# Kernel tuning notes

Hardware: AMD Instinct MI355X
Metric: run time of the kernel (lower is better)

## Reference

```python
import jax, jax.numpy as jnp
import numpy as np
import math

N, E, T, H, IN_DIM, G, L = 8192, 131072, 262144, 128, 64, 32, 2
RBF_BINS, RBF_MAX, ANG_BINS = 32, 5.0, 16


def _rbf(d, r_max, n_bins):
    centers = jnp.linspace(0.0, r_max, n_bins, dtype=jnp.float32)
    delta = r_max / max(n_bins - 1, 1)
    gamma = 1.0 / (2.0 * (delta ** 2 + 1e-12))
    diff = d[:, None] - centers[None, :]
    return jnp.exp(-gamma * diff * diff)


def _mlp2(x, w1, b1, w2, b2):
    return jax.nn.silu(x @ w1 + b1) @ w2 + b2


def _ln(x, g, b):
    mu = jnp.mean(x, -1, keepdims=True)
    var = jnp.mean((x - mu) ** 2, -1, keepdims=True)
    return (x - mu) * jax.lax.rsqrt(var + 1e-5) * g + b


def _safe_norm(v):
    # ||v|| with grad-safe sqrt at v=0
    return jnp.sqrt(jnp.sum(v * v, -1) + 1e-12)


def setup_inputs() -> dict:
    key = jax.random.key(0)
    ks = iter(jax.random.split(key, 64))

    def lin(fan_in, shape):
        return jax.random.normal(next(ks), shape, jnp.float32) * (fan_in ** -0.5)

    x = jax.random.normal(next(ks), (N, IN_DIM), jnp.float32)
    pos = jax.random.normal(next(ks), (N, 3), jnp.float32) * 2.0
    edge_index = jax.random.randint(next(ks), (2, E), 0, N, jnp.int32)
    edge_dist = jnp.linalg.norm(pos[edge_index[1]] - pos[edge_index[0]], axis=-1)
    triplet_kj = jax.random.randint(next(ks), (T,), 0, E, jnp.int32)
    triplet_ji = jax.random.randint(next(ks), (T,), 0, E, jnp.int32)
    batch = jnp.sort(jax.random.randint(next(ks), (N,), 0, G, jnp.int32))
    TM_IN, MM_IN, CTX = 2 * RBF_BINS + ANG_BINS, 3 * H + RBF_BINS, 3 * H
    d = dict(
        x=x, pos=pos, edge_dist=edge_dist,
        node_in_w=lin(IN_DIM, (IN_DIM, H)), node_in_b=jnp.zeros(H),
        tm_w1=lin(TM_IN, (L, TM_IN, H)), tm_b1=jnp.zeros((L, H)),
        tm_w2=lin(H, (L, H, H)), tm_b2=jnp.zeros((L, H)),
        mm_w1=lin(MM_IN, (L, MM_IN, H)), mm_b1=jnp.zeros((L, H)),
        mm_w2=lin(H, (L, H, 2 * H)), mm_b2=jnp.zeros((L, 2 * H)),
        us_w1=lin(CTX, (L, CTX, H)), us_b1=jnp.zeros((L, H)),
        us_w2=lin(H, (L, H, H)), us_b2=jnp.zeros((L, H)),
        gv_w1=lin(CTX, (L, CTX, H)), gv_b1=jnp.zeros((L, H)),
        gv_w2=lin(H, (L, H, H)), gv_b2=jnp.zeros((L, H)),
        ln_g=jnp.ones((L, H)), ln_b=jnp.zeros((L, H)),
        vn_init=jnp.zeros(H),
        v2n_w1=lin(H, (H, H)), v2n_b1=jnp.zeros(H),
        v2n_w2=lin(H, (H, H)), v2n_b2=jnp.zeros(H),
        n2v_w1=lin(H, (H, H)), n2v_b1=jnp.zeros(H),
        n2v_w2=lin(H, (H, H)), n2v_b2=jnp.zeros(H),
        head_w1=lin(5 * H, (5 * H, H)), head_b1=jnp.zeros(H),
        head_w2=lin(H, (H, 1)), head_b2=jnp.zeros(1),
        edge_index=edge_index, triplet_kj=triplet_kj,
        triplet_ji=triplet_ji, batch=batch,
    )
    return d


def reference(x, pos, edge_dist, node_in_w, node_in_b, tm_w1, tm_b1, tm_w2, tm_b2,
              mm_w1, mm_b1, mm_w2, mm_b2, us_w1, us_b1, us_w2, us_b2,
              gv_w1, gv_b1, gv_w2, gv_b2, ln_g, ln_b, vn_init,
              v2n_w1, v2n_b1, v2n_w2, v2n_b2, n2v_w1, n2v_b1, n2v_w2, n2v_b2,
              head_w1, head_b1, head_w2, head_b2,
              edge_index, triplet_kj, triplet_ji, batch):
    src, dst = edge_index[0], edge_index[1]
    s = x @ node_in_w + node_in_b                              # [N,H]
    v = jnp.zeros((N, H, 3), s.dtype)                          # [N,H,3]
    vec = pos[dst] - pos[src]                                  # [E,3]
    edge_dir = vec / (edge_dist[:, None] + 1e-9)               # [E,3]
    edge_rbf = _rbf(edge_dist, RBF_MAX, RBF_BINS)              # [E,32]
    # 3-body angles between edge ji and edge kj
    a, b = vec[triplet_ji], vec[triplet_kj]                    # [T,3]
    cos = jnp.sum(a * b, -1) / (_safe_norm(a) * _safe_norm(b) + 1e-9)
    angle = jnp.arccos(jnp.clip(cos, -1.0 + 1e-7, 1.0 - 1e-7))
    angle_feat = _rbf(angle, math.pi, ANG_BINS)                # [T,16]
    vn = jnp.broadcast_to(vn_init, (G, H))
    for l in range(L):
        s = s + _mlp2(vn, v2n_w1, v2n_b1, v2n_w2, v2n_b2)[batch]
        # triplet gather -> MLP -> scatter onto edges
        t_in = jnp.concatenate([edge_rbf[triplet_kj], edge_rbf[triplet_ji], angle_feat], -1)
        t_msg = _mlp2(t_in, tm_w1[l], tm_b1[l], tm_w2[l], tm_b2[l])
        angle_agg = jax.ops.segment_sum(t_msg, triplet_ji, num_segments=E)   # [E,H]
        # edge messages -> scatter onto nodes (scalar + vector channels)
        msg_in = jnp.concatenate([s[src], s[dst], edge_rbf, angle_agg], -1)  # [E,416]
        msg = _mlp2(msg_in, mm_w1[l], mm_b1[l], mm_w2[l], mm_b2[l])          # [E,2H]
        m_s, m_vc = msg[:, :H], msg[:, H:]
        agg_s = jax.ops.segment_sum(m_s, dst, num_segments=N)                # [N,H]
        m_v = m_vc[:, :, None] * edge_dir[:, None, :]                        # [E,H,3]
        agg_v = jax.ops.segment_sum(m_v.reshape(E, H * 3), dst, num_segments=N).reshape(N, H, 3)
        ctx = jnp.concatenate([s, agg_s, _safe_norm(v)], -1)                 # [N,3H]
        s = s + _mlp2(ctx, us_w1[l], us_b1[l], us_w2[l], us_b2[l])
        gate = jax.nn.sigmoid(_mlp2(ctx, gv_w1[l], gv_b1[l], gv_w2[l], gv_b2[l]))
        v = v + gate[:, :, None] * agg_v
        s = jax.nn.silu(_ln(s, ln_g[l], ln_b[l]))
        vn = vn + _mlp2(jax.ops.segment_sum(s, batch, num_segments=G),
                        n2v_w1, n2v_b1, n2v_w2, n2v_b2)
    nf = jnp.concatenate([s, _safe_norm(v)], -1)                             # [N,2H]
    add_p = jax.ops.segment_sum(nf, batch, num_segments=G)
    counts = jax.ops.segment_sum(jnp.ones((N,), nf.dtype), batch, num_segments=G)
    mean_p = add_p / jnp.maximum(counts, 1.0)[:, None]
    g = jnp.concatenate([add_p, mean_p, vn], -1)                             # [G,5H]
    pred = _mlp2(g, head_w1, head_b1, head_w2, head_b2)                      # [G,1]
    return pred[:, 0]
```

## Files before the change

kernel.cpp:

```cpp
#include <hip/hip_runtime.h>
#include <math.h>

#define N_   8192
#define E_   131072
#define T_   262144
#define H_   128
#define IND_ 64
#define G_   32
#define L_   2

#define CW 64
#define RB 16

#define MROWS 32
#define HSTRIDE 136
#define WSTRIDE 36

#define STEP_E  ((float)(5.0/31.0))
#define GAMMA_E ((float)(1.0/(2.0*((5.0/31.0)*(5.0/31.0) + 1e-12))))
#define PI_D    3.14159265358979323846
#define STEP_A  ((float)(PI_D/15.0))
#define GAMMA_A ((float)(1.0/(2.0*((PI_D/15.0)*(PI_D/15.0) + 1e-12))))

typedef __attribute__((ext_vector_type(8))) short short8;
typedef __attribute__((ext_vector_type(4))) float f32x4;
typedef unsigned short ushort_t;

static __device__ __forceinline__ float silu_f(float x){ return x / (1.f + expf(-x)); }
static __device__ __forceinline__ float sigmoid_f(float x){ return 1.f / (1.f + expf(-x)); }

static __device__ __forceinline__ ushort_t f2bf(float x){
  unsigned int u = __builtin_bit_cast(unsigned int, x);
  u += 0x7FFFu + ((u >> 16) & 1u);
  return (ushort_t)(u >> 16);
}
static __device__ __forceinline__ float bf2f(ushort_t h){
  unsigned int u = ((unsigned int)h) << 16;
  return __builtin_bit_cast(float, u);
}


__global__ void k_zero(float* __restrict__ p, long n){
  long stride = (long)gridDim.x*256;
  long n4 = n >> 2;
  float4* p4 = (float4*)p;
  for (long i = (long)blockIdx.x*256 + threadIdx.x; i < n4; i += stride)
    p4[i] = make_float4(0.f,0.f,0.f,0.f);
  for (long i = (n4<<2) + (long)blockIdx.x*256 + threadIdx.x; i < n; i += stride)
    p[i] = 0.f;
}

__global__ void k_sentinel(float* __restrict__ p, int n){
  int i = blockIdx.x*256 + threadIdx.x;
  if (i < n) p[i] = 1.0e30f;
}

__global__ void k_init_vn(float* __restrict__ vn, const float* __restrict__ vn_init){
  int i = blockIdx.x*256 + threadIdx.x;
  if (i < G_*H_) vn[i] = vn_init[i & 127];
}

__global__ void k_bhist(const int* __restrict__ batch, int* __restrict__ bh){
  int i = blockIdx.x*256 + threadIdx.x;
  if (i < N_) atomicAdd(&bh[batch[i]], 1);
}
__global__ void k_bscan(int* __restrict__ bh){
  if (threadIdx.x == 0 && blockIdx.x == 0){
    int a = 0;
    for (int g=0; g<G_; g++){ a += bh[g]; bh[g] = a; }
  }
}

__global__ void k_wt_all(const float* __restrict__ tm_w1, const float* __restrict__ tm_w2,
                         const float* __restrict__ mm_w1, const float* __restrict__ mm_w2,
                         const float* __restrict__ us_w1, const float* __restrict__ us_w2,
                         const float* __restrict__ gv_w1, const float* __restrict__ gv_w2,
                         ushort_t* __restrict__ wtbuf){
  const int l = blockIdx.y;
  int i = blockIdx.x*256 + threadIdx.x;
  if (i >= 245760) return;
  ushort_t* base = wtbuf + (size_t)l*376832;
  if (i < 12288){
    int c = i/96, k = i%96;
    base[i] = (k < 80) ? f2bf(tm_w1[(size_t)l*10240 + (size_t)k*128 + c]) : (ushort_t)0;
  } else if (i < 28672){
    int j = i - 12288; int c = j >> 7, k = j & 127;
    base[12288 + j] = f2bf(tm_w2[(size_t)l*16384 + (size_t)k*128 + c]);
  } else if (i < 81920){
    int j = i - 28672; int c = j/416, k = j%416;
    base[28672 + j] = f2bf(mm_w1[(size_t)l*53248 + (size_t)k*128 + c]);
  } else if (i < 114688){
    int j = i - 81920; int c = j >> 7, k = j & 127;
    base[81920 + j] = f2bf(mm_w2[(size_t)l*32768 + (size_t)k*256 + c]);
  } else if (i < 163840){
    int j = i - 114688; int c = j/384, k = j%384;
    float w = us_w1[(size_t)l*49152 + (size_t)k*128 + c];
    ushort_t h = f2bf(w);
    base[114688 + j] = h; base[163840 + j] = f2bf(w - bf2f(h));
  } else if (i < 180224){
    int j = i - 163840; int c = j >> 7, k = j & 127;
    float w = us_w2[(size_t)l*16384 + (size_t)k*128 + c];
    ushort_t h = f2bf(w);
    base[212992 + j] = h; base[229376 + j] = f2bf(w - bf2f(h));
  } else if (i < 229376){
    int j = i - 180224; int c = j/384, k = j%384;
    float w = gv_w1[(size_t)l*49152 + (size_t)k*128 + c];
    ushort_t h = f2bf(w);
    base[245760 + j] = h; base[294912 + j] = f2bf(w - bf2f(h));
  } else {
    int j = i - 229376; int c = j >> 7, k = j & 127;
    float w = gv_w2[(size_t)l*16384 + (size_t)k*128 + c];
    ushort_t h = f2bf(w);
    base[344064 + j] = h; base[360448 + j] = f2bf(w - bf2f(h));
  }
}

__global__ void k_geom(const float* __restrict__ pos, const float* __restrict__ dist,
                       const int* __restrict__ ei,
                       float* __restrict__ vec, float* __restrict__ dir,
                       ushort_t* __restrict__ rbf16){
  int e = blockIdx.x*256 + threadIdx.x;
  if (e >= E_) return;
  int s = ei[e], d = ei[E_ + e];
  float vx = pos[d*3+0] - pos[s*3+0];
  float vy = pos[d*3+1] - pos[s*3+1];
  float vz = pos[d*3+2] - pos[s*3+2];
  vec[e*3+0]=vx; vec[e*3+1]=vy; vec[e*3+2]=vz;
  float dd = dist[e];
  float inv = 1.f / (dd + 1e-9f);
  dir[e*3+0]=vx*inv; dir[e*3+1]=vy*inv; dir[e*3+2]=vz*inv;
  #pragma unroll
  for (int i=0;i<32;i++){
    float df = dd - i*STEP_E;
    rbf16[e*32+i] = f2bf(expf(-GAMMA_E*df*df));
  }
}

__global__ void k_dirs(const float* __restrict__ dir, const int* __restrict__ perm_e,
                       float* __restrict__ dir_s){
  int p = blockIdx.x*256 + threadIdx.x;
  if (p >= E_) return;
  int e = perm_e[p];
  dir_s[p*3+0] = dir[e*3+0];
  dir_s[p*3+1] = dir[e*3+1];
  dir_s[p*3+2] = dir[e*3+2];
}

__global__ void k_angle(const float* __restrict__ vec,
                        const int* __restrict__ kj, const int* __restrict__ ji,
                        float* __restrict__ angle){
  int t = blockIdx.x*256 + threadIdx.x;
  if (t >= T_) return;
  int ea = ji[t], eb = kj[t];
  float ax=vec[ea*3+0], ay=vec[ea*3+1], az=vec[ea*3+2];
  float bx=vec[eb*3+0], by=vec[eb*3+1], bz=vec[eb*3+2];
  float dot = ax*bx + ay*by + az*bz;
  float na = sqrtf(ax*ax+ay*ay+az*az + 1e-12f);
  float nb = sqrtf(bx*bx+by*by+bz*bz + 1e-12f);
  float c = dot / (na*nb + 1e-9f);
  c = fminf(fmaxf(c, -1.f + 1e-7f), 1.f - 1e-7f);
  angle[t] = acosf(c);
}


__global__ void k_hist(const int* __restrict__ keys, int M, int* __restrict__ hist){
  int i = blockIdx.x*256 + threadIdx.x;
  if (i < M) atomicAdd(&hist[keys[i]], 1);
}

__global__ void k_hist2(const int* __restrict__ keys, const int* __restrict__ map,
                        int M, int* __restrict__ hist){
  int i = blockIdx.x*256 + threadIdx.x;
  if (i < M) atomicAdd(&hist[map[keys[i]]], 1);
}

__global__ void k_scan1(const int* __restrict__ in, int* __restrict__ out,
                        int* __restrict__ sums, int B){
  __shared__ int sh[1024];
  int base = blockIdx.x*1024, t = threadIdx.x;
  for (int j=t;j<1024;j+=256) sh[j] = (base+j<B) ? in[base+j] : 0;
  __syncthreads();
  for (int o=1;o<1024;o<<=1){
    int v[4];
    #pragma unroll
    for (int q=0;q<4;q++){ int idx=t+q*256; v[q]=(idx>=o)? sh[idx-o]:0; }
    __syncthreads();
    #pragma unroll
    for (int q=0;q<4;q++){ int idx=t+q*256; sh[idx]+=v[q]; }
    __syncthreads();
  }
  for (int j=t;j<1024;j+=256) if (base+j<B) out[base+j] = (j==0)?0:sh[j-1];
  if (t==0) sums[blockIdx.x] = sh[1023];
}

__global__ void k_scan2(int* __restrict__ sums, int nb){
  if (threadIdx.x==0 && blockIdx.x==0){
    int a=0;
    for (int i=0;i<nb;i++){ int x=sums[i]; sums[i]=a; a+=x; }
  }
}

__global__ void k_scan3(int* __restrict__ out, const int* __restrict__ sums, int B){
  int i = blockIdx.x*256+threadIdx.x;
  if (i<B) out[i] += sums[i>>10];
}

__global__ void k_fill(const int* __restrict__ keys, int M, int* __restrict__ cur,
                       int* __restrict__ perm){
  int i = blockIdx.x*256+threadIdx.x;
  if (i<M){ int p = atomicAdd(&cur[keys[i]],1); perm[p]=i; }
}

__global__ void k_fill2(const int* __restrict__ keys, const int* __restrict__ map,
                        int M, int* __restrict__ cur, int* __restrict__ perm){
  int i = blockIdx.x*256+threadIdx.x;
  if (i<M){ int p = atomicAdd(&cur[map[keys[i]]],1); perm[p]=i; }
}

__global__ void k_invert(const int* __restrict__ perm, int* __restrict__ rank, int M){
  int i = blockIdx.x*256+threadIdx.x;
  if (i<M) rank[perm[i]] = i;
}

template<int SM, int K1PAD>
__launch_bounds__(256, 3)
__global__ void k_mlp1(
    const int* __restrict__ perm,
    const int* __restrict__ idx1, const int* __restrict__ idx2,
    const ushort_t* __restrict__ rbf16, const float* __restrict__ angle,
    const ushort_t* __restrict__ s16, const ushort_t* __restrict__ eagg_in,
    const ushort_t* __restrict__ W1t, const float* __restrict__ b1,
    ushort_t* __restrict__ outbuf)
{
  __shared__ ushort_t lw[128*WSTRIDE];
  __shared__ ushort_t hid[4*MROWS*HSTRIDE];
  const int tid  = threadIdx.x;
  const int wave = tid >> 6;
  const int lane = tid & 63;
  const int n    = lane & 15;
  const int quad = lane >> 4;
  const int kq   = quad*8;
  const int wrow = blockIdx.x*128 + wave*MROWS;
  ushort_t* myhid = hid + wave*MROWS*HSTRIDE;

  const int e0 = perm[wrow + n];
  const int e1 = perm[wrow + 16 + n];

  int i1a = idx1[e0], i1b = idx1[e1];
  int i2a = idx2[e0], i2b = idx2[e1];
  float ang0 = 0.f, ang1 = 0.f;
  if (SM == 1){ ang0 = angle[e0]; ang1 = angle[e1]; }

  f32x4 acc[2][8];
  #pragma unroll
  for (int rh=0;rh<2;rh++)
    #pragma unroll
    for (int ct=0;ct<8;ct++) acc[rh][ct] = (f32x4){0.f,0.f,0.f,0.f};

  #pragma unroll
  for (int k0 = 0; k0 < K1PAD; k0 += 32){
    #pragma unroll
    for (int it=0; it<2; it++){
      int idx = tid + it*256;
      int col = idx >> 2, seg = idx & 3;
      *(short8*)&lw[col*WSTRIDE + seg*8] = *(const short8*)&W1t[(size_t)col*K1PAD + k0 + seg*8];
    }
    __syncthreads();

    short8 a0, a1;
    if (SM == 1){
      if (k0 == 0){
        a0 = *(const short8*)&rbf16[(size_t)i1a*32 + kq];
        a1 = *(const short8*)&rbf16[(size_t)i1b*32 + kq];
      } else if (k0 == 32){
        a0 = *(const short8*)&rbf16[(size_t)i2a*32 + kq];
        a1 = *(const short8*)&rbf16[(size_t)i2b*32 + kq];
      } else {
        #pragma unroll
        for (int j=0;j<8;j++){
          int kk = kq + j;
          float v0 = 0.f, v1 = 0.f;
          if (kk < 16){
            float c = (float)kk*STEP_A;
            float d0 = ang0 - c, d1 = ang1 - c;
            v0 = expf(-GAMMA_A*d0*d0); v1 = expf(-GAMMA_A*d1*d1);
          }
          a0[j] = (short)f2bf(v0); a1[j] = (short)f2bf(v1);
        }
      }
    } else {
      const int k = k0 + kq;
      if (k0 < 128){
        a0 = *(const short8*)&s16[(size_t)i1a*128 + k];
        a1 = *(const short8*)&s16[(size_t)i1b*128 + k];
      } else if (k0 < 256){
        a0 = *(const short8*)&s16[(size_t)i2a*128 + (k-128)];
        a1 = *(const short8*)&s16[(size_t)i2b*128 + (k-128)];
      } else if (k0 < 288){
        a0 = *(const short8*)&rbf16[(size_t)e0*32 + (k-256)];
        a1 = *(const short8*)&rbf16[(size_t)e1*32 + (k-256)];
      } else {
        a0 = *(const short8*)&eagg_in[(size_t)(wrow + n)*128 + (k-288)];
        a1 = *(const short8*)&eagg_in[(size_t)(wrow + 16 + n)*128 + (k-288)];
      }
    }
    #pragma unroll
    for (int ct=0;ct<8;ct++){
      short8 b = *(const short8*)&lw[(ct*16 + n)*WSTRIDE + kq];
      acc[0][ct] = __builtin_amdgcn_mfma_f32_16x16x32_bf16(a0, b, acc[0][ct], 0,0,0);
      acc[1][ct] = __builtin_amdgcn_mfma_f32_16x16x32_bf16(a1, b, acc[1][ct], 0,0,0);
    }
    __syncthreads();
  }

  #pragma unroll
  for (int rh=0;rh<2;rh++){
    #pragma unroll
    for (int ct=0;ct<8;ct++){
      int col = ct*16 + n;
      float bv = b1[col];
      #pragma unroll
      for (int reg=0;reg<4;reg++){
        int rloc = rh*16 + quad*4 + reg;
        float h = acc[rh][ct][reg] + bv;
        myhid[rloc*HSTRIDE + col] = f2bf(silu_f(h));
      }
    }
  }
  const int rsub = lane >> 4;
  const int c8   = (lane & 15) * 8;
  #pragma unroll
  for (int i=0;i<8;i++){
    int rloc = i*4 + rsub;
    int grow = wrow + rloc;
    short8 vv = *(const short8*)&myhid[(size_t)rloc*HSTRIDE + c8];
    *(short8*)&outbuf[(size_t)grow*128 + c8] = vv;
  }
}

__global__ void k_agg_t(const ushort_t* __restrict__ tmsg, const int* __restrict__ tends,
                        ushort_t* __restrict__ eagg2){
  int i = blockIdx.x*256 + threadIdx.x;
  int r = i >> 6, c2 = (i & 63)*2;
  if (r >= E_) return;
  int s = (r == 0) ? 0 : tends[r-1];
  int e = tends[r];
  float a0 = 0.f, a1 = 0.f;
  for (int p=s;p<e;p++){
    unsigned int w = *(const unsigned int*)&tmsg[(size_t)p*128 + c2];
    a0 += bf2f((ushort_t)(w & 0xFFFFu));
    a1 += bf2f((ushort_t)(w >> 16));
  }
  unsigned int o = (unsigned int)f2bf(a0) | ((unsigned int)f2bf(a1) << 16);
  *(unsigned int*)&eagg2[(size_t)r*128 + c2] = o;
}

__global__ void k_agg_e(const ushort_t* __restrict__ hbuf, const int* __restrict__ eends,
                        const float* __restrict__ dir_s, float* __restrict__ mom){
  int i = blockIdx.x*256 + threadIdx.x;
  int d = i >> 6, c2 = (i & 63)*2;
  if (d >= N_) return;
  int s = (d == 0) ? 0 : eends[d-1];
  int e = eends[d];
  float hs0=0.f,hs1=0.f, hx0=0.f,hx1=0.f, hy0=0.f,hy1=0.f, hz0=0.f,hz1=0.f;
  float sdx=0.f, sdy=0.f, sdz=0.f;
  for (int q=s;q<e;q++){
    unsigned int w = *(const unsigned int*)&hbuf[(size_t)q*128 + c2];
    float h0 = bf2f((ushort_t)(w & 0xFFFFu));
    float h1 = bf2f((ushort_t)(w >> 16));
    float dx = dir_s[q*3+0], dy = dir_s[q*3+1], dz = dir_s[q*3+2];
    hs0 += h0; hs1 += h1;
    hx0 += h0*dx; hx1 += h1*dx;
    hy0 += h0*dy; hy1 += h1*dy;
    hz0 += h0*dz; hz1 += h1*dz;
    sdx += dx; sdy += dy; sdz += dz;
  }
  size_t base = (size_t)d*128 + c2;
  *(float2*)&mom[base]                        = make_float2(hs0, hs1);
  *(float2*)&mom[(size_t)N_*128   + base]     = make_float2(hx0, hx1);
  *(float2*)&mom[(size_t)N_*256   + base]     = make_float2(hy0, hy1);
  *(float2*)&mom[(size_t)N_*384   + base]     = make_float2(hz0, hz1);
  if (c2 == 0){
    mom[(size_t)N_*512 + d*4+0] = sdx;
    mom[(size_t)N_*512 + d*4+1] = sdy;
    mom[(size_t)N_*512 + d*4+2] = sdz;
  }
}

__launch_bounds__(64, 4)
__global__ void k_gemm_t(ushort_t* __restrict__ eagg2, const int* __restrict__ tends,
                         const ushort_t* __restrict__ W2t, const float* __restrict__ b2){
  __shared__ ushort_t hid[MROWS*HSTRIDE];
  const int lane = threadIdx.x;
  const int n    = lane & 15;
  const int quad = lane >> 4;
  const int kq   = quad*8;
  const int wrow = blockIdx.x*MROWS;

  f32x4 acc[2][8];
  #pragma unroll
  for (int rh=0;rh<2;rh++)
    #pragma unroll
    for (int ct=0;ct<8;ct++) acc[rh][ct] = (f32x4){0.f,0.f,0.f,0.f};

  #pragma unroll
  for (int k0=0;k0<128;k0+=32){
    short8 a0 = *(const short8*)&eagg2[(size_t)(wrow + n)*128 + k0 + kq];
    short8 a1 = *(const short8*)&eagg2[(size_t)(wrow + 16 + n)*128 + k0 + kq];
    #pragma unroll
    for (int ct=0;ct<8;ct++){
      short8 b = *(const short8*)&W2t[(size_t)(ct*16 + n)*128 + k0 + kq];
      acc[0][ct] = __builtin_amdgcn_mfma_f32_16x16x32_bf16(a0, b, acc[0][ct], 0,0,0);
      acc[1][ct] = __builtin_amdgcn_mfma_f32_16x16x32_bf16(a1, b, acc[1][ct], 0,0,0);
    }
  }

  float cnts[2][4];
  #pragma unroll
  for (int rh=0;rh<2;rh++)
    #pragma unroll
    for (int reg=0;reg<4;reg++){
      int row = wrow + rh*16 + quad*4 + reg;
      cnts[rh][reg] = (float)(tends[row] - (row ? tends[row-1] : 0));
    }

  #pragma unroll
  for (int rh=0;rh<2;rh++){
    #pragma unroll
    for (int ct=0;ct<8;ct++){
      int col = ct*16 + n;
      float bv = b2[col];
      #pragma unroll
      for (int reg=0;reg<4;reg++){
        int rloc = rh*16 + quad*4 + reg;
        hid[rloc*HSTRIDE + col] = f2bf(acc[rh][ct][reg] + cnts[rh][reg]*bv);
      }
    }
  }
  const int rsub = lane >> 4;
  const int c8   = (lane & 15) * 8;
  #pragma unroll
  for (int i=0;i<8;i++){
    int rloc = i*4 + rsub;
    int grow = wrow + rloc;
    short8 vv = *(const short8*)&hid[(size_t)rloc*HSTRIDE + c8];
    *(short8*)&eagg2[(size_t)grow*128 + c8] = vv;
  }
}

__launch_bounds__(64, 4)
__global__ void k_gemm_e(const float* __restrict__ mom, const int* __restrict__ eends,
                         const ushort_t* __restrict__ W2t ,
                         const float* __restrict__ b2 ,
                         const float* __restrict__ v ,
                         ushort_t* __restrict__ a16h, ushort_t* __restrict__ a16l,
                         ushort_t* __restrict__ vnh,  ushort_t* __restrict__ vnl,
                         float* __restrict__ aggv ){
  __shared__ float sbuf[MROWS*130];
  const int lane = threadIdx.x;
  const int n    = lane & 15;
  const int quad = lane >> 4;
  const int kq   = quad*8;
  const int wrow = blockIdx.x*MROWS;
  const int og   = blockIdx.y;

  const float* M = mom + (size_t)og*((size_t)N_*128);
  const ushort_t* W = W2t + (og ? (size_t)128*128 : 0);

  f32x4 acc[2][8];
  #pragma unroll
  for (int rh=0;rh<2;rh++)
    #pragma unroll
    for (int ct=0;ct<8;ct++) acc[rh][ct] = (f32x4){0.f,0.f,0.f,0.f};

  #pragma unroll
  for (int k0=0;k0<128;k0+=32){
    const int k = k0 + kq;
    const float* p0 = &M[(size_t)(wrow + n)*128 + k];
    const float* p1 = &M[(size_t)(wrow + 16 + n)*128 + k];
    f32x4 x0 = *(const f32x4*)p0, x1 = *(const f32x4*)(p0+4);
    f32x4 y0 = *(const f32x4*)p1, y1 = *(const f32x4*)(p1+4);
    short8 ah0, al0, ah1, al1;
    #pragma unroll
    for (int j=0;j<4;j++){
      ushort_t h;
      h = f2bf(x0[j]); ah0[j]   = (short)h; al0[j]   = (short)f2bf(x0[j] - bf2f(h));
      h = f2bf(x1[j]); ah0[4+j] = (short)h; al0[4+j] = (short)f2bf(x1[j] - bf2f(h));
      h = f2bf(y0[j]); ah1[j]   = (short)h; al1[j]   = (short)f2bf(y0[j] - bf2f(h));
      h = f2bf(y1[j]); ah1[4+j] = (short)h; al1[4+j] = (short)f2bf(y1[j] - bf2f(h));
    }
    #pragma unroll
    for (int ct=0;ct<8;ct++){
      short8 b = *(const short8*)&W[(size_t)(ct*16 + n)*128 + k0 + kq];
      acc[0][ct] = __builtin_amdgcn_mfma_f32_16x16x32_bf16(ah0, b, acc[0][ct], 0,0,0);
      acc[0][ct] = __builtin_amdgcn_mfma_f32_16x16x32_bf16(al0, b, acc[0][ct], 0,0,0);
      acc[1][ct] = __builtin_amdgcn_mfma_f32_16x16x32_bf16(ah1, b, acc[1][ct], 0,0,0);
      acc[1][ct] = __builtin_amdgcn_mfma_f32_16x16x32_bf16(al1, b, acc[1][ct], 0,0,0);
    }
  }

  const int rsub = lane >> 4;
  const int c8   = (lane & 15) * 8;

  if (og == 0){
    float cnts[2][4];
    #pragma unroll
    for (int rh=0;rh<2;rh++)
      #pragma unroll
      for (int reg=0;reg<4;reg++){
        int row = wrow + rh*16 + quad*4 + reg;
        cnts[rh][reg] = (float)(eends[row] - (row ? eends[row-1] : 0));
      }
    ushort_t* us = (ushort_t*)sbuf;
    #pragma unroll
    for (int rh=0;rh<2;rh++)
      #pragma unroll
      for (int ct=0;ct<8;ct++){
        int col = ct*16 + n;
        float bv = b2[col];
        #pragma unroll
        for (int reg=0;reg<4;reg++){
          int rloc = rh*16 + quad*4 + reg;
          float val = acc[rh][ct][reg] + cnts[rh][reg]*bv;
          us[rloc*HSTRIDE + col] = f2bf(val);
        }
      }
    #pragma unroll
    for (int i=0;i<8;i++){
      int rloc = i*4 + rsub;
      short8 vv = *(const short8*)&us[(size_t)rloc*HSTRIDE + c8];
      *(short8*)&a16h[(size_t)(wrow + rloc)*128 + c8] = vv;
    }
    #pragma unroll
    for (int rh=0;rh<2;rh++)
      #pragma unroll
      for (int ct=0;ct<8;ct++){
        int col = ct*16 + n;
        float bv = b2[col];
        #pragma unroll
        for (int reg=0;reg<4;reg++){
          int rloc = rh*16 + quad*4 + reg;
          float val = acc[rh][ct][reg] + cnts[rh][reg]*bv;
          ushort_t h = f2bf(val);
          us[rloc*HSTRIDE + col] = f2bf(val - bf2f(h));
        }
      }
    #pragma unroll
    for (int i=0;i<8;i++){
      int rloc = i*4 + rsub;
      short8 vv = *(const short8*)&us[(size_t)rloc*HSTRIDE + c8];
      *(short8*)&a16l[(size_t)(wrow + rloc)*128 + c8] = vv;
    }
    #pragma unroll 4
    for (int j=0;j<32;j++){
      size_t idx = (size_t)wrow*128 + (size_t)j*128 + lane*2;
      float2 a = *(const float2*)&v[idx];
      float2 b = *(const float2*)&v[(size_t)N_*128 + idx];
      float2 c = *(const float2*)&v[(size_t)N_*256 + idx];
      float n0 = sqrtf(a.x*a.x + b.x*b.x + c.x*c.x + 1e-12f);
      float n1 = sqrtf(a.y*a.y + b.y*b.y + c.y*c.y + 1e-12f);
      ushort_t h0 = f2bf(n0), h1 = f2bf(n1);
      *(unsigned int*)&vnh[idx] = (unsigned int)h0 | ((unsigned int)h1 << 16);
      *(unsigned int*)&vnl[idx] = (unsigned int)f2bf(n0 - bf2f(h0))
                                | ((unsigned int)f2bf(n1 - bf2f(h1)) << 16);
    }
  } else {
    const int x = og - 1;
    #pragma unroll
    for (int rh=0;rh<2;rh++)
      #pragma unroll
      for (int ct=0;ct<8;ct++){
        int col = ct*16 + n;
        float bv = b2[128 + col];
        #pragma unroll
        for (int reg=0;reg<4;reg++){
          int rloc = rh*16 + quad*4 + reg;
          int row = wrow + rloc;
          float sd = mom[(size_t)N_*512 + row*4 + x];
          sbuf[rloc*130 + col] = acc[rh][ct][reg] + sd*bv;
        }
      }
    float* plane = aggv + (size_t)x*((size_t)N_*128);
    #pragma unroll
    for (int i=0;i<8;i++){
      int rloc = i*4 + rsub;
      f32x4 v0 = *(const f32x4*)&sbuf[rloc*130 + c8];
      f32x4 v1 = *(const f32x4*)&sbuf[rloc*130 + c8 + 4];
      *(f32x4*)&plane[(size_t)(wrow + rloc)*128 + c8] = v0;
      *(f32x4*)&plane[(size_t)(wrow + rloc)*128 + c8 + 4] = v1;
    }
  }
}

__launch_bounds__(256, 3)
__global__ void k_node_mfma(
    const float* __restrict__ s_in,
    const ushort_t* __restrict__ a16h, const ushort_t* __restrict__ a16l,
    const ushort_t* __restrict__ vnh,  const ushort_t* __restrict__ vnl,
    float* __restrict__ s2, float* __restrict__ v_out ,
    const float* __restrict__ aggv ,
    const ushort_t* __restrict__ us1h, const ushort_t* __restrict__ us1l, const float* __restrict__ us_b1,
    const ushort_t* __restrict__ us2h, const ushort_t* __restrict__ us2l, const float* __restrict__ us_b2,
    const ushort_t* __restrict__ gv1h, const ushort_t* __restrict__ gv1l, const float* __restrict__ gv_b1,
    const ushort_t* __restrict__ gv2h, const ushort_t* __restrict__ gv2l, const float* __restrict__ gv_b2)
{
  __shared__ ushort_t lwh[128*WSTRIDE];
  __shared__ ushort_t lwl[128*WSTRIDE];
  __shared__ ushort_t hidh[4][16*HSTRIDE];
  __shared__ ushort_t hidl[4][16*HSTRIDE];
  const int tid  = threadIdx.x;
  const int wave = tid >> 6;
  const int lane = tid & 63;
  const int n    = lane & 15;
  const int quad = lane >> 4;
  const int kq   = quad*8;
  const int og   = blockIdx.y;
  const int wrow = blockIdx.x*64 + wave*16;
  const int r0 = wrow + n;

  const ushort_t* W1h = og ? gv1h : us1h;
  const ushort_t* W1l = og ? gv1l : us1l;
  const float*    B1  = og ? gv_b1 : us_b1;
  const ushort_t* W2h = og ? gv2h : us2h;
  const ushort_t* W2l = og ? gv2l : us2l;
  const float*    B2  = og ? gv_b2 : us_b2;

  f32x4 acc[8];
  #pragma unroll
  for (int ct=0;ct<8;ct++) acc[ct] = (f32x4){0.f,0.f,0.f,0.f};

  #pragma unroll
  for (int k0=0; k0<384; k0+=32){
    #pragma unroll
    for (int it = 0; it < 2; it++){
      int idx = tid + it*256;
      int col = idx >> 2, seg = idx & 3;
      *(short8*)&lwh[col*WSTRIDE + seg*8] = *(const short8*)&W1h[(size_t)col*384 + k0 + seg*8];
      *(short8*)&lwl[col*WSTRIDE + seg*8] = *(const short8*)&W1l[(size_t)col*384 + k0 + seg*8];
    }
    __syncthreads();

    short8 ah0, al0;
    const int k = k0 + kq;
    if (k0 < 128){
      const float* p0 = &s_in[(size_t)r0*128 + k];
      f32x4 x0 = *(const f32x4*)p0, x1 = *(const f32x4*)(p0+4);
      #pragma unroll
      for (int j=0;j<4;j++){
        ushort_t h;
        h = f2bf(x0[j]); ah0[j]   = (short)h; al0[j]   = (short)f2bf(x0[j] - bf2f(h));
        h = f2bf(x1[j]); ah0[4+j] = (short)h; al0[4+j] = (short)f2bf(x1[j] - bf2f(h));
      }
    } else if (k0 < 256){
      int kk = k - 128;
      ah0 = *(const short8*)&a16h[(size_t)r0*128 + kk];
      al0 = *(const short8*)&a16l[(size_t)r0*128 + kk];
    } else {
      int kk = k - 256;
      ah0 = *(const short8*)&vnh[(size_t)r0*128 + kk];
      al0 = *(const short8*)&vnl[(size_t)r0*128 + kk];
    }
    #pragma unroll
    for (int ct=0;ct<8;ct++){
      short8 bh = *(const short8*)&lwh[(ct*16 + n)*WSTRIDE + kq];
      short8 bl = *(const short8*)&lwl[(ct*16 + n)*WSTRIDE + kq];
      acc[ct] = __builtin_amdgcn_mfma_f32_16x16x32_bf16(ah0, bh, acc[ct], 0,0,0);
      acc[ct] = __builtin_amdgcn_mfma_f32_16x16x32_bf16(al0, bh, acc[ct], 0,0,0);
      acc[ct] = __builtin_amdgcn_mfma_f32_16x16x32_bf16(ah0, bl, acc[ct], 0,0,0);
    }
    __syncthreads();
  }

  #pragma unroll
  for (int ct=0;ct<8;ct++){
    int col = ct*16 + n;
    float bv = B1[col];
    #pragma unroll
    for (int reg=0;reg<4;reg++){
      int rloc = quad*4 + reg;
      float h = silu_f(acc[ct][reg] + bv);
      ushort_t hh = f2bf(h);
      hidh[wave][rloc*HSTRIDE + col] = hh;
      hidl[wave][rloc*HSTRIDE + col] = f2bf(h - bf2f(hh));
    }
  }

  f32x4 acc2[8];
  #pragma unroll
  for (int ct=0;ct<8;ct++) acc2[ct] = (f32x4){0.f,0.f,0.f,0.f};

  #pragma unroll
  for (int k0=0;k0<128;k0+=32){
    #pragma unroll
    for (int it = 0; it < 2; it++){
      int idx = tid + it*256;
      int col = idx >> 2, seg = idx & 3;
      *(short8*)&lwh[col*WSTRIDE + seg*8] = *(const short8*)&W2h[(size_t)col*128 + k0 + seg*8];
      *(short8*)&lwl[col*WSTRIDE + seg*8] = *(const short8*)&W2l[(size_t)col*128 + k0 + seg*8];
    }
    __syncthreads();

    short8 ah0 = *(const short8*)&hidh[wave][(size_t)(n)*HSTRIDE + k0 + kq];
    short8 al0 = *(const short8*)&hidl[wave][(size_t)(n)*HSTRIDE + k0 + kq];
    #pragma unroll
    for (int ct=0;ct<8;ct++){
      short8 bh = *(const short8*)&lwh[(ct*16 + n)*WSTRIDE + kq];
      short8 bl = *(const short8*)&lwl[(ct*16 + n)*WSTRIDE + kq];
      acc2[ct] = __builtin_amdgcn_mfma_f32_16x16x32_bf16(ah0, bh, acc2[ct], 0,0,0);
      acc2[ct] = __builtin_amdgcn_mfma_f32_16x16x32_bf16(al0, bh, acc2[ct], 0,0,0);
      acc2[ct] = __builtin_amdgcn_mfma_f32_16x16x32_bf16(ah0, bl, acc2[ct], 0,0,0);
    }
    __syncthreads();
  }

  if (og == 0){
    #pragma unroll
    for (int ct=0;ct<8;ct++){
      int col = ct*16 + n;
      float bv = B2[col];
      #pragma unroll
      for (int reg=0;reg<4;reg++){
        int row = wrow + quad*4 + reg;
        size_t idx = (size_t)row*128 + col;
        s2[idx] = s_in[idx] + acc2[ct][reg] + bv;
      }
    }
  } else {
    #pragma unroll
    for (int ct=0;ct<8;ct++){
      int col = ct*16 + n;
      float bv = B2[col];
      #pragma unroll
      for (int reg=0;reg<4;reg++){
        int row = wrow + quad*4 + reg;
        size_t idx = (size_t)row*128 + col;
        float g = sigmoid_f(acc2[ct][reg] + bv);
        v_out[idx]                    += g*aggv[idx];
        v_out[(size_t)N_*128 + idx]   += g*aggv[(size_t)N_*128 + idx];
        v_out[(size_t)N_*256 + idx]   += g*aggv[(size_t)N_*256 + idx];
      }
    }
  }
}

__launch_bounds__(128)
__global__ void k_gemm(const float* __restrict__ A,
                       const float* __restrict__ W,
                       const float* __restrict__ bias,
                       float* __restrict__ C, int R, int K)
{
  __shared__ float ws[CW*128];
  __shared__ float as[RB][CW];
  const int tid = threadIdx.x;
  const int nchunk = (K + CW - 1) / CW;

  for (int rb = blockIdx.x*RB; rb < R; rb += gridDim.x*RB){
    float acc[RB];
    #pragma unroll
    for (int r=0;r<RB;r++) acc[r] = 0.f;

    for (int c=0;c<nchunk;c++){
      const int k0 = c*CW;
      for (int i=tid; i<CW*128; i+=128){
        int kk = i >> 7, col = i & 127;
        int k = k0 + kk;
        ws[i] = (k < K) ? W[k*128 + col] : 0.f;
      }
      for (int i=tid; i<RB*CW; i+=128){
        int r  = i >> 6, kk = i & 63;
        int k  = k0 + kk;
        as[r][kk] = (k < K) ? A[(long)(rb+r)*K + k] : 0.f;
      }
      __syncthreads();
      #pragma unroll 4
      for (int kq2=0; kq2<CW/4; kq2++){
        float w0 = ws[(4*kq2+0)*128 + tid];
        float w1 = ws[(4*kq2+1)*128 + tid];
        float w2 = ws[(4*kq2+2)*128 + tid];
        float w3 = ws[(4*kq2+3)*128 + tid];
        #pragma unroll
        for (int r=0;r<RB;r++){
          const float4 av = *reinterpret_cast<const float4*>(&as[r][4*kq2]);
          acc[r] = fmaf(av.x, w0, acc[r]);
          acc[r] = fmaf(av.y, w1, acc[r]);
          acc[r] = fmaf(av.z, w2, acc[r]);
          acc[r] = fmaf(av.w, w3, acc[r]);
        }
      }
      __syncthreads();
    }

    const float bv = bias[tid];
    #pragma unroll
    for (int r=0;r<RB;r++)
      C[(long)(rb+r)*128 + tid] = acc[r] + bv;
  }
}


__launch_bounds__(256)
__global__ void k_small_mlp2(const float* __restrict__ in,
                             const float* __restrict__ w1, const float* __restrict__ b1,
                             const float* __restrict__ w2, const float* __restrict__ b2,
                             float* __restrict__ outp, int accumulate){
  __shared__ float a[32][128];
  __shared__ float h[32][128];
  int tid = threadIdx.x;
  for (int i=tid;i<32*128;i+=256) a[i>>7][i&127] = in[i];
  __syncthreads();
  int col = tid & 127, rg = tid >> 7;
  float acc[16];
  #pragma unroll
  for (int r=0;r<16;r++) acc[r]=0.f;
  for (int k=0;k<128;k++){
    float w = w1[k*128+col];
    #pragma unroll
    for (int r=0;r<16;r++) acc[r] = fmaf(a[rg*16+r][k], w, acc[r]);
  }
  {
    float bv = b1[col];
    #pragma unroll
    for (int r=0;r<16;r++) h[rg*16+r][col] = silu_f(acc[r]+bv);
  }
  __syncthreads();
  #pragma unroll
  for (int r=0;r<16;r++) acc[r]=0.f;
  for (int k=0;k<128;k++){
    float w = w2[k*128+col];
    #pragma unroll
    for (int r=0;r<16;r++) acc[r] = fmaf(h[rg*16+r][k], w, acc[r]);
  }
  {
    float bv = b2[col];
    #pragma unroll
    for (int r=0;r<16;r++){
      int idx = (rg*16+r)*128+col;
      float val = acc[r]+bv;
      outp[idx] = accumulate ? outp[idx]+val : val;
    }
  }
}

__global__ void k_head(const float* __restrict__ gbuf,
                       const float* __restrict__ w1, const float* __restrict__ b1,
                       const float* __restrict__ w2, const float* __restrict__ b2,
                       float* __restrict__ outp){
  __shared__ float red[128];
  int g = blockIdx.x, tid = threadIdx.x;
  float acc = 0.f;
  for (int k=0;k<640;k++) acc = fmaf(gbuf[g*640+k], w1[k*128+tid], acc);
  float h = silu_f(acc + b1[tid]);
  red[tid] = h * w2[tid];
  __syncthreads();
  for (int o=64;o>0;o>>=1){ if (tid<o) red[tid]+=red[tid+o]; __syncthreads(); }
  if (tid == 0) outp[g] = red[0] + b2[0];
}


__global__ void k_sadd_batch(float* __restrict__ s, const float* __restrict__ t2,
                             const int* __restrict__ batch, ushort_t* __restrict__ s16){
  int i = blockIdx.x*256 + threadIdx.x;
  if (i >= N_*H_) return;
  int n = i >> 7, h = i & 127;
  float v = s[i] + t2[batch[n]*128 + h];
  s[i] = v;
  s16[i] = f2bf(v);
}

__global__ void k_ln_silu(const float* __restrict__ in, float* __restrict__ outp,
                          const float* __restrict__ g, const float* __restrict__ b){
  __shared__ float red[128];
  int n = blockIdx.x, tid = threadIdx.x;
  float x = in[n*128 + tid];
  red[tid] = x; __syncthreads();
  for (int o=64;o>0;o>>=1){ if (tid<o) red[tid]+=red[tid+o]; __syncthreads(); }
  float mu = red[0] * (1.f/128.f);
  __syncthreads();
  float dx = x - mu;
  red[tid] = dx*dx; __syncthreads();
  for (int o=64;o>0;o>>=1){ if (tid<o) red[tid]+=red[tid+o]; __syncthreads(); }
  float var = red[0] * (1.f/128.f);
  float y = dx * rsqrtf(var + 1e-5f) * g[tid] + b[tid];
  outp[n*128 + tid] = silu_f(y);
}

__global__ void k_ssum_csr(const float* __restrict__ s, const int* __restrict__ bends,
                           float* __restrict__ ssum){
  int g = blockIdx.x, c = blockIdx.y, tid = threadIdx.x;
  int s0 = g ? bends[g-1] : 0;
  int e0 = bends[g];
  long len = e0 - s0;
  int lo = s0 + (int)((len*c) >> 3);
  int hi = s0 + (int)((len*(c+1)) >> 3);
  float a = 0.f;
  for (int n=lo; n<hi; n++) a += s[(size_t)n*128 + tid];
  if (hi > lo) atomicAdd(&ssum[g*128 + tid], a);
}

__global__ void k_scatter_nf2(const float* __restrict__ s, const float* __restrict__ v ,
                              const int* __restrict__ batch, float* __restrict__ addp){
  int j = threadIdx.x;
  int base = blockIdx.x*32;
  float acc = 0.f;
  int prev = batch[base];
  for (int r=0;r<32;r++){
    int nn = base + r;
    int b = batch[nn];
    if (b != prev){ atomicAdd(&addp[prev*256 + j], acc); acc = 0.f; prev = b; }
    float val;
    if (j < 128){
      val = s[(size_t)nn*128 + j];
    } else {
      size_t idx = (size_t)nn*128 + (j - 128);
      float v0 = v[idx], v1 = v[(size_t)N_*128 + idx], v2 = v[(size_t)N_*256 + idx];
      val = sqrtf(v0*v0 + v1*v1 + v2*v2 + 1e-12f);
    }
    acc += val;
  }
  atomicAdd(&addp[prev*256 + j], acc);
}

__global__ void k_build_g(const float* __restrict__ addp, const int* __restrict__ bends,
                          const float* __restrict__ vn, float* __restrict__ gbuf){
  int i = blockIdx.x*256 + threadIdx.x;
  if (i >= G_*640) return;
  int g = i / 640, j = i % 640;
  float cnt = (float)(bends[g] - (g ? bends[g-1] : 0));
  float val;
  if (j < 256)       val = addp[g*256 + j];
  else if (j < 512)  val = addp[g*256 + (j-256)] / fmaxf(cnt, 1.f);
  else               val = vn[g*128 + (j-512)];
  gbuf[i] = val;
}


extern "C" void kernel_launch(void* const* d_in, const int* in_sizes, int n_in,
                              void* d_out, int out_size, void* d_ws, size_t ws_size,
                              hipStream_t stream)
{
  const float* x         = (const float*)d_in[0];
  const float* pos       = (const float*)d_in[1];
  const float* edist     = (const float*)d_in[2];
  const float* node_in_w = (const float*)d_in[3];
  const float* node_in_b = (const float*)d_in[4];
  const float* tm_w1 = (const float*)d_in[5];
  const float* tm_b1 = (const float*)d_in[6];
  const float* tm_w2 = (const float*)d_in[7];
  const float* tm_b2 = (const float*)d_in[8];
  const float* mm_w1 = (const float*)d_in[9];
  const float* mm_b1 = (const float*)d_in[10];
  const float* mm_w2 = (const float*)d_in[11];
  const float* mm_b2 = (const float*)d_in[12];
  const float* us_w1 = (const float*)d_in[13];
  const float* us_b1 = (const float*)d_in[14];
  const float* us_w2 = (const float*)d_in[15];
  const float* us_b2 = (const float*)d_in[16];
  const float* gv_w1 = (const float*)d_in[17];
  const float* gv_b1 = (const float*)d_in[18];
  const float* gv_w2 = (const float*)d_in[19];
  const float* gv_b2 = (const float*)d_in[20];
  const float* ln_g  = (const float*)d_in[21];
  const float* ln_b  = (const float*)d_in[22];
  const float* vn_init = (const float*)d_in[23];
  const float* v2n_w1 = (const float*)d_in[24];
  const float* v2n_b1 = (const float*)d_in[25];
  const float* v2n_w2 = (const float*)d_in[26];
  const float* v2n_b2 = (const float*)d_in[27];
  const float* n2v_w1 = (const float*)d_in[28];
  const float* n2v_b1 = (const float*)d_in[29];
  const float* n2v_w2 = (const float*)d_in[30];
  const float* n2v_b2 = (const float*)d_in[31];
  const float* head_w1 = (const float*)d_in[32];
  const float* head_b1 = (const float*)d_in[33];
  const float* head_w2 = (const float*)d_in[34];
  const float* head_b2 = (const float*)d_in[35];
  const int* ei    = (const int*)d_in[36];
  const int* t_kj  = (const int*)d_in[37];
  const int* t_ji  = (const int*)d_in[38];
  const int* batch = (const int*)d_in[39];
  float* out = (float*)d_out;

  float* f = (float*)d_ws;
  size_t off = 0;
  auto alloc = [&](size_t n){ n = (n + 3) & ~(size_t)3; float* p = f + off; off += n; return p; };
  float*    vec    = alloc((size_t)E_*3);
  float*    dir    = alloc((size_t)E_*3);
  ushort_t* rbf16  = (ushort_t*)alloc((size_t)E_*16);
  float*    angle  = alloc((size_t)T_);
  float*    tmsg_f = alloc((size_t)E_*128);
  float*    eagg2_f= alloc((size_t)E_*64);
  float*    dir_s  = alloc((size_t)E_*3);
  float*    tends_f= alloc((size_t)E_ + 1024);
  float*    eends_f= alloc((size_t)N_ + 1024);
  float*    bends_f= alloc((size_t)G_);
  float*    s      = alloc((size_t)N_*128);
  ushort_t* s16    = (ushort_t*)alloc((size_t)N_*64);
  float*    v      = alloc((size_t)N_*384);
  float*    aggv   = alloc((size_t)N_*384);
  float*    rank_f = alloc((size_t)E_);
  float*    wtbuf_f= alloc((size_t)376832);
  float*    vn     = alloc((size_t)G_*128);
  float*    tg2    = alloc((size_t)G_*128);
  float*    ssum   = alloc((size_t)G_*128);
  float*    addp   = alloc((size_t)G_*256);
  float*    gbuf   = alloc((size_t)G_*640);

  if (off * sizeof(float) > ws_size){
    k_sentinel<<<1, 64, 0, stream>>>(out, G_);
    return;
  }

  int* perm_t = (int*)vec;
  int* perm_e = perm_t + T_;
  int* rank_e = (int*)rank_f;
  int* tends  = (int*)tends_f;
  int* eends  = (int*)eends_f;
  int* bends  = (int*)bends_f;
  ushort_t* tmsg   = (ushort_t*)tmsg_f;
  ushort_t* ehid   = (ushort_t*)tmsg_f;
  ushort_t* eagg2  = (ushort_t*)eagg2_f;
  float*    mom  = eagg2_f;
  ushort_t* a16h = (ushort_t*)(eagg2_f + 4227072);
  ushort_t* a16l = a16h + (size_t)N_*128;
  ushort_t* vnh  = a16l + (size_t)N_*128;
  ushort_t* vnl  = vnh  + (size_t)N_*128;
  float*    s2   = (float*)(vnl + (size_t)N_*128);

  ushort_t* wtbuf = (ushort_t*)wtbuf_f;
  auto WT = [&](int l, size_t o){ return wtbuf + (size_t)l*376832 + o; };

  auto zero = [&](float* p, long n){
    int blocks = (int)((n/4 + 255)/256); if (blocks > 16384) blocks = 16384; if (blocks < 1) blocks = 1;
    k_zero<<<blocks, 256, 0, stream>>>(p, n);
  };
  auto csort = [&](const int* keys, const int* map, int M, int B, int* perm, int* ends){
    int nb = (B+1023)/1024;
    zero((float*)ends, B + nb);
    if (map) k_hist2<<<(M+255)/256, 256, 0, stream>>>(keys, map, M, ends);
    else     k_hist <<<(M+255)/256, 256, 0, stream>>>(keys, M, ends);
    k_scan1<<<nb, 256, 0, stream>>>(ends, ends, ends + B, B);
    k_scan2<<<1, 64, 0, stream>>>(ends + B, nb);
    k_scan3<<<(B+255)/256, 256, 0, stream>>>(ends, ends + B, B);
    if (map) k_fill2<<<(M+255)/256, 256, 0, stream>>>(keys, map, M, ends, perm);
    else     k_fill <<<(M+255)/256, 256, 0, stream>>>(keys, M, ends, perm);
  };

  zero(v, (long)N_*384);
  k_init_vn<<<(G_*H_ + 255)/256, 256, 0, stream>>>(vn, vn_init);
  k_geom<<<(E_ + 255)/256, 256, 0, stream>>>(pos, edist, ei, vec, dir, rbf16);
  k_angle<<<(T_ + 255)/256, 256, 0, stream>>>(vec, t_kj, t_ji, angle);
  csort(ei+E_, nullptr, E_, N_, perm_e, eends);
  k_invert<<<(E_+255)/256, 256, 0, stream>>>(perm_e, rank_e, E_);
  k_dirs<<<(E_+255)/256, 256, 0, stream>>>(dir, perm_e, dir_s);
  csort(t_ji, rank_e, T_, E_, perm_t, tends);
  zero(bends_f, G_);
  k_bhist<<<(N_+255)/256, 256, 0, stream>>>(batch, bends);
  k_bscan<<<1, 64, 0, stream>>>(bends);
  k_wt_all<<<dim3(960, 2), 256, 0, stream>>>(tm_w1, tm_w2, mm_w1, mm_w2,
                                             us_w1, us_w2, gv_w1, gv_w2, wtbuf);
  k_gemm<<<512, 128, 0, stream>>>(x, node_in_w, node_in_b, s, N_, IND_);

  for (int l=0; l<L_; l++){
    k_small_mlp2<<<1, 256, 0, stream>>>(vn, v2n_w1, v2n_b1, v2n_w2, v2n_b2, tg2, 0);
    k_sadd_batch<<<(N_*H_ + 255)/256, 256, 0, stream>>>(s, tg2, batch, s16);

    k_mlp1<1,96><<<T_/128, 256, 0, stream>>>(perm_t, t_kj, t_ji,
        rbf16, angle, s16, eagg2, WT(l,0), tm_b1 + l*128, tmsg);
    k_agg_t<<<(E_*64)/256, 256, 0, stream>>>(tmsg, tends, eagg2);
    k_gemm_t<<<E_/MROWS, 64, 0, stream>>>(eagg2, tends, WT(l,12288), tm_b2 + l*128);

    k_mlp1<2,416><<<E_/128, 256, 0, stream>>>(perm_e, ei, ei + E_,
        rbf16, angle, s16, eagg2, WT(l,28672), mm_b1 + l*128, ehid);
    k_agg_e<<<(N_*64)/256, 256, 0, stream>>>(ehid, eends, dir_s, mom);
    k_gemm_e<<<dim3(N_/MROWS, 4), 64, 0, stream>>>(mom, eends, WT(l,81920), mm_b2 + l*256,
        v, a16h, a16l, vnh, vnl, aggv);

    k_node_mfma<<<dim3(N_/64, 2), 256, 0, stream>>>(s, a16h, a16l, vnh, vnl, s2, v, aggv,
        WT(l,114688), WT(l,163840), us_b1 + l*128, WT(l,212992), WT(l,229376), us_b2 + l*128,
        WT(l,245760), WT(l,294912), gv_b1 + l*128, WT(l,344064), WT(l,360448), gv_b2 + l*128);

    k_ln_silu<<<N_, 128, 0, stream>>>(s2, s, ln_g + l*128, ln_b + l*128);
    zero(ssum, (long)G_*128);
    k_ssum_csr<<<dim3(G_, 8), 128, 0, stream>>>(s, bends, ssum);
    k_small_mlp2<<<1, 256, 0, stream>>>(ssum, n2v_w1, n2v_b1, n2v_w2, n2v_b2, vn, 1);
  }

  zero(addp, (long)G_*256);
  k_scatter_nf2<<<N_/32, 256, 0, stream>>>(s, v, batch, addp);
  k_build_g<<<(G_*640 + 255)/256, 256, 0, stream>>>(addp, bends, vn, gbuf);
  k_head<<<G_, 128, 0, stream>>>(gbuf, head_w1, head_b1, head_w2, head_b2, out);
}
```

Before: 945.8 us.

## Fuse triplet aggregation into edge GEMM and parallelize small MLP across blocks

Merges the triplet-to-edge segment sum into the following MFMA GEMM kernel, so each block sums its rows' triplet messages in registers before the matrix multiply. This removes one launch and the write and re-read of the intermediate aggregate buffer. Each lane now walks a variable-length segment serially, which may cause divergence and uncoalesced gathers. Separately, the tiny 32-row MLP is split across 8 blocks of 4 rows each instead of one block, cutting its serial latency.

```diff
diff --git a/kernel.cpp b/kernel.cpp
--- a/kernel.cpp
+++ b/kernel.cpp
@@ -338,21 +338,88 @@
   }
 }
 
-__global__ void k_agg_t(const ushort_t* __restrict__ tmsg, const int* __restrict__ tends,
-                        ushort_t* __restrict__ eagg2){
-  int i = blockIdx.x*256 + threadIdx.x;
-  int r = i >> 6, c2 = (i & 63)*2;
-  if (r >= E_) return;
-  int s = (r == 0) ? 0 : tends[r-1];
-  int e = tends[r];
-  float a0 = 0.f, a1 = 0.f;
-  for (int p=s;p<e;p++){
-    unsigned int w = *(const unsigned int*)&tmsg[(size_t)p*128 + c2];
-    a0 += bf2f((ushort_t)(w & 0xFFFFu));
-    a1 += bf2f((ushort_t)(w >> 16));
-  }
-  unsigned int o = (unsigned int)f2bf(a0) | ((unsigned int)f2bf(a1) << 16);
-  *(unsigned int*)&eagg2[(size_t)r*128 + c2] = o;
+__launch_bounds__(64, 4)
+__global__ void k_aggemm_t(const ushort_t* __restrict__ tmsg, const int* __restrict__ tends,
+                           const ushort_t* __restrict__ W2t, const float* __restrict__ b2,
+                           ushort_t* __restrict__ eagg2){
+  __shared__ ushort_t hid[MROWS*HSTRIDE];
+  const int lane = threadIdx.x;
+  const int n    = lane & 15;
+  const int quad = lane >> 4;
+  const int kq   = quad*8;
+  const int wrow = blockIdx.x*MROWS;
+  const int r0 = wrow + n, r1 = wrow + 16 + n;
+  const int s0 = r0 ? tends[r0-1] : 0;
+  const int e0 = tends[r0];
+  const int s1 = tends[r1-1];
+  const int e1 = tends[r1];
+
+  f32x4 acc[2][8];
+  #pragma unroll
+  for (int rh=0;rh<2;rh++)
+    #pragma unroll
+    for (int ct=0;ct<8;ct++) acc[rh][ct] = (f32x4){0.f,0.f,0.f,0.f};
+
+  #pragma unroll
+  for (int k0=0;k0<128;k0+=32){
+    float sum0[8], sum1[8];
+    #pragma unroll
+    for (int j=0;j<8;j++){ sum0[j]=0.f; sum1[j]=0.f; }
+    for (int p=s0;p<e0;p++){
+      short8 w = *(const short8*)&tmsg[(size_t)p*128 + k0 + kq];
+      #pragma unroll
+      for (int j=0;j<8;j++) sum0[j] += bf2f((ushort_t)w[j]);
+    }
+    for (int p=s1;p<e1;p++){
+      short8 w = *(const short8*)&tmsg[(size_t)p*128 + k0 + kq];
+      #pragma unroll
+      for (int j=0;j<8;j++) sum1[j] += bf2f((ushort_t)w[j]);
+    }
+    short8 a0, a1;
+    #pragma unroll
+    for (int j=0;j<8;j++){
+      a0[j] = (short)f2bf(sum0[j]);
+      a1[j] = (short)f2bf(sum1[j]);
+    }
+    #pragma unroll
+    for (int ct=0;ct<8;ct++){
+      short8 b = *(const short8*)&W2t[(size_t)(ct*16 + n)*128 + k0 + kq];
+      acc[0][ct] = __builtin_amdgcn_mfma_f32_16x16x32_bf16(a0, b, acc[0][ct], 0,0,0);
+      acc[1][ct] = __builtin_amdgcn_mfma_f32_16x16x32_bf16(a1, b, acc[1][ct], 0,0,0);
+    }
+  }
+
+  float cnts[2][4];
+  #pragma unroll
+  for (int rh=0;rh<2;rh++)
+    #pragma unroll
+    for (int reg=0;reg<4;reg++){
+      int row = wrow + rh*16 + quad*4 + reg;
+      cnts[rh][reg] = (float)(tends[row] - (row ? tends[row-1] : 0));
+    }
+
+  #pragma unroll
+  for (int rh=0;rh<2;rh++){
+    #pragma unroll
+    for (int ct=0;ct<8;ct++){
+      int col = ct*16 + n;
+      float bv = b2[col];
+      #pragma unroll
+      for (int reg=0;reg<4;reg++){
+        int rloc = rh*16 + quad*4 + reg;
+        hid[rloc*HSTRIDE + col] = f2bf(acc[rh][ct][reg] + cnts[rh][reg]*bv);
+      }
+    }
+  }
+  const int rsub = lane >> 4;
+  const int c8   = (lane & 15) * 8;
+  #pragma unroll
+  for (int i=0;i<8;i++){
+    int rloc = i*4 + rsub;
+    int grow = wrow + rloc;
+    short8 vv = *(const short8*)&hid[(size_t)rloc*HSTRIDE + c8];
+    *(short8*)&eagg2[(size_t)grow*128 + c8] = vv;
+  }
 }
 
 __global__ void k_agg_e(const ushort_t* __restrict__ hbuf, const int* __restrict__ eends,
@@ -384,67 +451,6 @@
     mom[(size_t)N_*512 + d*4+0] = sdx;
     mom[(size_t)N_*512 + d*4+1] = sdy;
     mom[(size_t)N_*512 + d*4+2] = sdz;
-  }
-}
-
-__launch_bounds__(64, 4)
-__global__ void k_gemm_t(ushort_t* __restrict__ eagg2, const int* __restrict__ tends,
-                         const ushort_t* __restrict__ W2t, const float* __restrict__ b2){
-  __shared__ ushort_t hid[MROWS*HSTRIDE];
-  const int lane = threadIdx.x;
-  const int n    = lane & 15;
-  const int quad = lane >> 4;
-  const int kq   = quad*8;
-  const int wrow = blockIdx.x*MROWS;
-
-  f32x4 acc[2][8];
-  #pragma unroll
-  for (int rh=0;rh<2;rh++)
-    #pragma unroll
-    for (int ct=0;ct<8;ct++) acc[rh][ct] = (f32x4){0.f,0.f,0.f,0.f};
-
-  #pragma unroll
-  for (int k0=0;k0<128;k0+=32){
-    short8 a0 = *(const short8*)&eagg2[(size_t)(wrow + n)*128 + k0 + kq];
-    short8 a1 = *(const short8*)&eagg2[(size_t)(wrow + 16 + n)*128 + k0 + kq];
-    #pragma unroll
-    for (int ct=0;ct<8;ct++){
-      short8 b = *(const short8*)&W2t[(size_t)(ct*16 + n)*128 + k0 + kq];
-      acc[0][ct] = __builtin_amdgcn_mfma_f32_16x16x32_bf16(a0, b, acc[0][ct], 0,0,0);
-      acc[1][ct] = __builtin_amdgcn_mfma_f32_16x16x32_bf16(a1, b, acc[1][ct], 0,0,0);
-    }
-  }
-
-  float cnts[2][4];
-  #pragma unroll
-  for (int rh=0;rh<2;rh++)
-    #pragma unroll
-    for (int reg=0;reg<4;reg++){
-      int row = wrow + rh*16 + quad*4 + reg;
-      cnts[rh][reg] = (float)(tends[row] - (row ? tends[row-1] : 0));
-    }
-
-  #pragma unroll
-  for (int rh=0;rh<2;rh++){
-    #pragma unroll
-    for (int ct=0;ct<8;ct++){
-      int col = ct*16 + n;
-      float bv = b2[col];
-      #pragma unroll
-      for (int reg=0;reg<4;reg++){
-        int rloc = rh*16 + quad*4 + reg;
-        hid[rloc*HSTRIDE + col] = f2bf(acc[rh][ct][reg] + cnts[rh][reg]*bv);
-      }
-    }
-  }
-  const int rsub = lane >> 4;
-  const int c8   = (lane & 15) * 8;
-  #pragma unroll
-  for (int i=0;i<8;i++){
-    int rloc = i*4 + rsub;
-    int grow = wrow + rloc;
-    short8 vv = *(const short8*)&hid[(size_t)rloc*HSTRIDE + c8];
-    *(short8*)&eagg2[(size_t)grow*128 + c8] = vv;
   }
 }
 
@@ -803,41 +809,38 @@
                              const float* __restrict__ w1, const float* __restrict__ b1,
                              const float* __restrict__ w2, const float* __restrict__ b2,
                              float* __restrict__ outp, int accumulate){
-  __shared__ float a[32][128];
-  __shared__ float h[32][128];
+  __shared__ float a[4][128];
+  __shared__ float h[4][128];
   int tid = threadIdx.x;
-  for (int i=tid;i<32*128;i+=256) a[i>>7][i&127] = in[i];
+  int rbase = blockIdx.x*4;
+  for (int i=tid;i<4*128;i+=256) a[i>>7][i&127] = in[(rbase + (i>>7))*128 + (i&127)];
   __syncthreads();
   int col = tid & 127, rg = tid >> 7;
-  float acc[16];
-  #pragma unroll
-  for (int r=0;r<16;r++) acc[r]=0.f;
+  float acc0=0.f, acc1=0.f;
   for (int k=0;k<128;k++){
     float w = w1[k*128+col];
-    #pragma unroll
-    for (int r=0;r<16;r++) acc[r] = fmaf(a[rg*16+r][k], w, acc[r]);
+    acc0 = fmaf(a[rg*2+0][k], w, acc0);
+    acc1 = fmaf(a[rg*2+1][k], w, acc1);
   }
   {
     float bv = b1[col];
-    #pragma unroll
-    for (int r=0;r<16;r++) h[rg*16+r][col] = silu_f(acc[r]+bv);
+    h[rg*2+0][col] = silu_f(acc0+bv);
+    h[rg*2+1][col] = silu_f(acc1+bv);
   }
   __syncthreads();
-  #pragma unroll
-  for (int r=0;r<16;r++) acc[r]=0.f;
+  acc0=0.f; acc1=0.f;
   for (int k=0;k<128;k++){
     float w = w2[k*128+col];
-    #pragma unroll
-    for (int r=0;r<16;r++) acc[r] = fmaf(h[rg*16+r][k], w, acc[r]);
+    acc0 = fmaf(h[rg*2+0][k], w, acc0);
+    acc1 = fmaf(h[rg*2+1][k], w, acc1);
   }
   {
     float bv = b2[col];
-    #pragma unroll
-    for (int r=0;r<16;r++){
-      int idx = (rg*16+r)*128+col;
-      float val = acc[r]+bv;
-      outp[idx] = accumulate ? outp[idx]+val : val;
-    }
+    int idx0 = (rbase+rg*2+0)*128+col;
+    int idx1 = (rbase+rg*2+1)*128+col;
+    float v0 = acc0+bv, v1 = acc1+bv;
+    outp[idx0] = accumulate ? outp[idx0]+v0 : v0;
+    outp[idx1] = accumulate ? outp[idx1]+v1 : v1;
   }
 }
 
@@ -1061,13 +1064,12 @@
   k_gemm<<<512, 128, 0, stream>>>(x, node_in_w, node_in_b, s, N_, IND_);
 
   for (int l=0; l<L_; l++){
-    k_small_mlp2<<<1, 256, 0, stream>>>(vn, v2n_w1, v2n_b1, v2n_w2, v2n_b2, tg2, 0);
+    k_small_mlp2<<<8, 256, 0, stream>>>(vn, v2n_w1, v2n_b1, v2n_w2, v2n_b2, tg2, 0);
     k_sadd_batch<<<(N_*H_ + 255)/256, 256, 0, stream>>>(s, tg2, batch, s16);
 
     k_mlp1<1,96><<<T_/128, 256, 0, stream>>>(perm_t, t_kj, t_ji,
         rbf16, angle, s16, eagg2, WT(l,0), tm_b1 + l*128, tmsg);
-    k_agg_t<<<(E_*64)/256, 256, 0, stream>>>(tmsg, tends, eagg2);
-    k_gemm_t<<<E_/MROWS, 64, 0, stream>>>(eagg2, tends, WT(l,12288), tm_b2 + l*128);
+    k_aggemm_t<<<E_/MROWS, 64, 0, stream>>>(tmsg, tends, WT(l,12288), tm_b2 + l*128, eagg2);
 
     k_mlp1<2,416><<<E_/128, 256, 0, stream>>>(perm_e, ei, ei + E_,
         rbf16, angle, s16, eagg2, WT(l,28672), mm_b1 + l*128, ehid);
@@ -1082,7 +1084,7 @@
     k_ln_silu<<<N_, 128, 0, stream>>>(s2, s, ln_g + l*128, ln_b + l*128);
     zero(ssum, (long)G_*128);
     k_ssum_csr<<<dim3(G_, 8), 128, 0, stream>>>(s, bends, ssum);
-    k_small_mlp2<<<1, 256, 0, stream>>>(ssum, n2v_w1, n2v_b1, n2v_w2, n2v_b2, vn, 1);
+    k_small_mlp2<<<8, 256, 0, stream>>>(ssum, n2v_w1, n2v_b1, n2v_w2, n2v_b2, vn, 1);
   }
 
   zero(addp, (long)G_*256);
```

Result: faster. 866.1 us (-8.4%).
